# Performance work log

Measured on AMD Instinct MI355X. Metric: run time of the kernel, lower is better.

Reference implementation:

```python
import jax, jax.numpy as jnp
import numpy as np
import math

B, N, D, H = 2, 2048, 1024, 16
HD = D // H          # head dim = 64
ROT = 32             # rotary dim (applied to first ROT channels of each head)


def rotate_half(x):
    # '... (d r) -> ... d r' with r=2: even/odd interleaved pairs
    x1 = x[..., 0::2]
    x2 = x[..., 1::2]
    return jnp.stack((-x2, x1), axis=-1).reshape(x.shape)


def apply_rotary_pos_emb(t, freqs):
    rot_dim, seq_len = freqs.shape[-1], t.shape[-2]
    freqs = freqs[-seq_len:, :]
    t_rot, t_pass = t[..., :rot_dim], t[..., rot_dim:]
    t_rot = t_rot * jnp.cos(freqs) + rotate_half(t_rot) * jnp.sin(freqs)
    return jnp.concatenate((t_rot, t_pass), axis=-1)


def setup_inputs() -> dict:
    key = jax.random.key(0)
    ks = jax.random.split(key, 8)
    return {
        "q": jax.random.normal(ks[0], (B, N, D), jnp.float32),
        "k": jax.random.normal(ks[1], (B, N, D), jnp.float32),
        "v": jax.random.normal(ks[2], (B, N, D), jnp.float32),
        "wq": jax.random.normal(ks[3], (D, D), jnp.float32) * (1.0 / math.sqrt(D)),
        "wk": jax.random.normal(ks[4], (D, D), jnp.float32) * (1.0 / math.sqrt(D)),
        "wv": jax.random.normal(ks[5], (D, D), jnp.float32) * (1.0 / math.sqrt(D)),
        "wo": jax.random.normal(ks[6], (D, D), jnp.float32) * (1.0 / math.sqrt(D)),
        "rot_pos_emb": jax.random.normal(ks[7], (N, ROT), jnp.float32),
    }


def reference(q, k, v, wq, wk, wv, wo, rot_pos_emb):
    # projections (nn.Linear with bias=False: x @ W.T)
    qh = (q @ wq.T).reshape(B, N, H, HD).transpose(0, 2, 1, 3)  # b h n d
    kh = (k @ wk.T).reshape(B, N, H, HD).transpose(0, 2, 1, 3)
    vh = (v @ wv.T).reshape(B, N, H, HD).transpose(0, 2, 1, 3)
    qh = apply_rotary_pos_emb(qh, rot_pos_emb)
    kh = apply_rotary_pos_emb(kh, rot_pos_emb)
    k_t = kh.transpose(0, 1, 3, 2)                               # b h d n
    scores = (qh @ k_t) / math.sqrt(HD)                          # b h n n
    attn = jax.nn.softmax(scores, axis=-1)
    out = attn @ vh                                              # b h n d
    out = out.transpose(0, 2, 1, 3).reshape(B, N, H * HD)        # b n (h d)
    return (out @ wo.T, k_t, vh)
```

## Files before the change

### kernel.cpp

```cpp
#include <hip/hip_runtime.h>
#include <math.h>

#define NN 2048
#define DD 1024
#define HH 16
#define OUTSZ (2*NN*DD)

typedef unsigned short u16;
typedef unsigned int u32;
typedef __attribute__((ext_vector_type(8))) short short8;
typedef __attribute__((ext_vector_type(4))) float floatx4;
typedef __attribute__((ext_vector_type(4))) unsigned short us4;

__device__ __forceinline__ u16 f2bf(float x) {
    union { float f; unsigned u; } v; v.f = x;
    unsigned r = v.u + 0x7FFFu + ((v.u >> 16) & 1u);
    return (u16)(r >> 16);
}

__device__ __forceinline__ u32 fbits(float x) {
    union { float f; u32 u; } v; v.f = x; return v.u;
}

__device__ __forceinline__ u32 pack_bf2(float lo, float hi) {
    return __builtin_amdgcn_perm(fbits(hi) + 0x8000u, fbits(lo) + 0x8000u, 0x07060302u);
}

__device__ __forceinline__ float fexp2(float x) {
#if __has_builtin(__builtin_amdgcn_exp2f)
    return __builtin_amdgcn_exp2f(x);
#else
    return __expf(x * 0.69314718056f);
#endif
}

__device__ __forceinline__ void gl_lds16(const u16* g, u16* l) {
    __builtin_amdgcn_global_load_lds(
        (const __attribute__((address_space(1))) unsigned int*)g,
        (__attribute__((address_space(3))) unsigned int*)l, 16, 0, 0);
}

struct CastArgs { const float* s[7]; u16* d[7]; int n[7]; };

__global__ __launch_bounds__(256)
void cast_bf16(CastArgs a) {
    const int ten = blockIdx.y;
    const float4* s = (const float4*)a.s[ten];
    us4* d = (us4*)a.d[ten];
    const int n4 = a.n[ten] >> 2;
    for (int i = blockIdx.x * 256 + threadIdx.x; i < n4; i += gridDim.x * 256) {
        float4 f = s[i];
        us4 u = {f2bf(f.x), f2bf(f.y), f2bf(f.z), f2bf(f.w)};
        d[i] = u;
    }
}

struct ProjArgs {
    const u16* X[4]; const u16* W[4];
    float* outf[4];  u16* outb[4];
    const float* rot;
};

template<int TN>
__global__ __launch_bounds__(256)
void mfma_proj(ProjArgs a, int mode_base)
{
    constexpr int TNW = TN / 2;
    constexpr int NJ  = TNW / 16;

    __shared__ __align__(16) u16 As[128 * 64];
    __shared__ __align__(16) u16 Bs[TN * 64];

    const int mode = mode_base + blockIdx.z;
    const u16* __restrict__ X   = a.X[mode];
    const u16* __restrict__ Wm  = a.W[mode];
    float* __restrict__ outf    = a.outf[mode];
    u16* __restrict__ outb      = a.outb[mode];
    const float* __restrict__ rot = a.rot;

    const int t    = threadIdx.x;
    const int lane = t & 63;
    const int w    = t >> 6;
    const int wr   = (w >> 1) * 64;
    const int wc   = (w & 1) * TNW;
    const int m0   = blockIdx.y * 128;
    const int j0   = blockIdx.x * TN;

    const int lc = (t & 7) ^ ((t >> 3) & 7);
    const u16* gA = X  + (size_t)(m0 + (t >> 3)) * DD + lc * 8;
    const u16* gB = Wm + (size_t)(j0 + (t >> 3)) * DD + lc * 8;

    const int fr = lane & 15;
    const int fq = lane >> 4;

    floatx4 acc[4][NJ] = {};

    for (int k0 = 0; k0 < DD; k0 += 64) {
        __syncthreads();
        #pragma unroll
        for (int p = 0; p < 4; ++p)
            gl_lds16(gA + (size_t)(32 * p) * DD + k0, As + (p * 256 + t) * 8);
        #pragma unroll
        for (int p = 0; p < TN / 32; ++p)
            gl_lds16(gB + (size_t)(32 * p) * DD + k0, Bs + (p * 256 + t) * 8);
        __syncthreads();
        #pragma unroll
        for (int kk = 0; kk < 2; ++kk) {
            const int ph = (kk * 4 + fq) ^ (fr & 7);
            short8 af[4], bf[NJ];
            #pragma unroll
            for (int i = 0; i < 4; ++i)
                af[i] = *(const short8*)(As + (wr + i * 16 + fr) * 64 + ph * 8);
            #pragma unroll
            for (int j = 0; j < NJ; ++j)
                bf[j] = *(const short8*)(Bs + (wc + j * 16 + fr) * 64 + ph * 8);
            #pragma unroll
            for (int i = 0; i < 4; ++i)
                #pragma unroll
                for (int j = 0; j < NJ; ++j)
                    acc[i][j] = __builtin_amdgcn_mfma_f32_16x16x32_bf16(af[i], bf[j], acc[i][j], 0, 0, 0);
        }
    }

    const int b = m0 >> 11;
    #pragma unroll
    for (int i = 0; i < 4; ++i) {
        const int mrow  = m0 + wr + i * 16 + fq * 4;
        const int nbase = mrow & (NN - 1);
        #pragma unroll
        for (int j = 0; j < NJ; ++j) {
            const int col = j0 + wc + j * 16 + fr;
            const int h = col >> 6, d = col & 63;
            const int bh = b * HH + h;
            float v[4];
            #pragma unroll
            for (int r = 0; r < 4; ++r) v[r] = acc[i][j][r];
            if (mode <= 1 && ((wc + j * 16) & 63) < 32) {
                #pragma unroll
                for (int r = 0; r < 4; ++r) {
                    const int n = nbase + r;
                    float c = v[r];
                    float p = __shfl_xor(c, 1);
                    float f = rot[n * 32 + d];
                    float sn, cs; __sincosf(f, &sn, &cs);
                    v[r] = (d & 1) ? fmaf(c, cs, p * sn) : fmaf(c, cs, -p * sn);
                }
            }
            if (mode == 0) {
                #pragma unroll
                for (int r = 0; r < 4; ++r)
                    outb[((size_t)bh * NN + nbase + r) * 64 + d] = f2bf(v[r] * 0.1803368801111244f);
            } else if (mode == 1) {
                float4 f4 = {v[0], v[1], v[2], v[3]};
                *(float4*)&outf[((size_t)bh * 64 + d) * NN + nbase] = f4;
                #pragma unroll
                for (int r = 0; r < 4; ++r)
                    outb[((size_t)bh * NN + nbase + r) * 64 + d] = f2bf(v[r]);
            } else if (mode == 2) {
                #pragma unroll
                for (int r = 0; r < 4; ++r)
                    outf[((size_t)bh * NN + nbase + r) * 64 + d] = v[r];
                us4 u = {f2bf(v[0]), f2bf(v[1]), f2bf(v[2]), f2bf(v[3])};
                *(us4*)&outb[((size_t)bh * 64 + d) * NN + nbase] = u;
            } else {
                #pragma unroll
                for (int r = 0; r < 4; ++r)
                    outf[(size_t)(mrow + r) * DD + col] = v[r];
            }
        }
    }
}

__global__ __launch_bounds__(256)
void mfma_attn(const u16* __restrict__ qh, const u16* __restrict__ kh,
               const u16* __restrict__ vt, u16* __restrict__ ctx)
{
    __shared__ __align__(16) u16 Ks[64 * 64];
    __shared__ __align__(16) u16 Vs[64 * 64];
    __shared__ __align__(16) u16 Ps[4 * 32 * 64];

    const int t    = threadIdx.x;
    const int lane = t & 63;
    const int w    = t >> 6;
    const int fr   = lane & 15;
    const int fq   = lane >> 4;
    const int bh   = blockIdx.y;
    const int q0   = blockIdx.x * 128;
    const int b    = bh >> 4, h = bh & 15;

    short8 qf[2][2];
    #pragma unroll
    for (int c = 0; c < 2; ++c)
        #pragma unroll
        for (int kk = 0; kk < 2; ++kk)
            qf[c][kk] = *(const short8*)(qh +
                ((size_t)bh * NN + q0 + w * 32 + c * 16 + fr) * 64 + kk * 32 + fq * 8);

    const int lc = (t & 7) ^ ((t >> 3) & 7);
    const u16* kg = kh + ((size_t)bh * NN + (t >> 3)) * 64 + lc * 8;
    const u16* vg = vt + ((size_t)bh * 64 + (t >> 3)) * NN + lc * 8;
    u16* kl0 = Ks + t * 8;      u16* kl1 = Ks + (256 + t) * 8;
    u16* vl0 = Vs + t * 8;      u16* vl1 = Vs + (256 + t) * 8;

    u16* Prow0 = Ps + (w * 32 + fr) * 64;
    const int psw = 2 * (fr & 7);

    floatx4 o4[2][4] = {};
    float lrun[2] = {0.f, 0.f};

    for (int j0k = 0; j0k < NN; j0k += 64) {
        __syncthreads();
        gl_lds16(kg + (size_t)j0k * 64, kl0);
        gl_lds16(kg + (size_t)(j0k + 32) * 64, kl1);
        gl_lds16(vg + j0k, vl0);
        gl_lds16(vg + j0k + (size_t)32 * NN, vl1);
        __syncthreads();

        short8 kf[4][2];
        #pragma unroll
        for (int j = 0; j < 4; ++j)
            #pragma unroll
            for (int kk = 0; kk < 2; ++kk) {
                const int row = j * 16 + fr;
                const int phys = (kk * 4 + fq) ^ (row & 7);
                kf[j][kk] = *(const short8*)(Ks + row * 64 + phys * 8);
            }
        floatx4 sT[2][4] = {};
        #pragma unroll
        for (int c = 0; c < 2; ++c)
            #pragma unroll
            for (int j = 0; j < 4; ++j)
                #pragma unroll
                for (int kk = 0; kk < 2; ++kk)
                    sT[c][j] = __builtin_amdgcn_mfma_f32_16x16x32_bf16(kf[j][kk], qf[c][kk], sT[c][j], 0, 0, 0);

        #pragma unroll
        for (int c = 0; c < 2; ++c) {
            u16* pb = Prow0 + c * 16 * 64;
            #pragma unroll
            for (int j = 0; j < 4; ++j) {
                float p0 = fexp2(sT[c][j][0]);
                float p1 = fexp2(sT[c][j][1]);
                float p2 = fexp2(sT[c][j][2]);
                float p3 = fexp2(sT[c][j][3]);
                lrun[c] += (p0 + p1) + (p2 + p3);
                u32 lo = pack_bf2(p0, p1);
                u32 hi = pack_bf2(p2, p3);
                const int phys = (4 * j + fq) ^ psw;
                uint2 pv = {lo, hi};
                *(uint2*)(pb + phys * 4) = pv;
            }
        }

        short8 pa[2][2], vf[4][2];
        #pragma unroll
        for (int c = 0; c < 2; ++c)
            #pragma unroll
            for (int kk = 0; kk < 2; ++kk) {
                const int phys0 = (8 * kk + 2 * fq) ^ psw;
                pa[c][kk] = *(const short8*)(Prow0 + c * 16 * 64 + phys0 * 4);
            }
        #pragma unroll
        for (int n = 0; n < 4; ++n)
            #pragma unroll
            for (int kk = 0; kk < 2; ++kk) {
                const int row = n * 16 + fr;
                const int phys = (kk * 4 + fq) ^ (row & 7);
                vf[n][kk] = *(const short8*)(Vs + row * 64 + phys * 8);
            }
        #pragma unroll
        for (int c = 0; c < 2; ++c)
            #pragma unroll
            for (int n = 0; n < 4; ++n)
                #pragma unroll
                for (int kk = 0; kk < 2; ++kk)
                    o4[c][n] = __builtin_amdgcn_mfma_f32_16x16x32_bf16(pa[c][kk], vf[n][kk], o4[c][n], 0, 0, 0);
    }

    #pragma unroll
    for (int c = 0; c < 2; ++c) {
        lrun[c] += __shfl_xor(lrun[c], 16);
        lrun[c] += __shfl_xor(lrun[c], 32);
    }

    #pragma unroll
    for (int c = 0; c < 2; ++c)
        #pragma unroll
        for (int r = 0; r < 4; ++r) {
            const float inv = 1.0f / __shfl(lrun[c], fq * 4 + r);
            const int qrow = q0 + w * 32 + c * 16 + fq * 4 + r;
            const size_t base = ((size_t)b * NN + qrow) * DD + h * 64 + fr;
            #pragma unroll
            for (int n = 0; n < 4; ++n)
                ctx[base + n * 16] = f2bf(o4[c][n][r] * inv);
        }
}

extern "C" void kernel_launch(void* const* d_in, const int* in_sizes, int n_in,
                              void* d_out, int out_size, void* d_ws, size_t ws_size,
                              hipStream_t stream)
{
    const float* q   = (const float*)d_in[0];
    const float* k   = (const float*)d_in[1];
    const float* v   = (const float*)d_in[2];
    const float* wq  = (const float*)d_in[3];
    const float* wk  = (const float*)d_in[4];
    const float* wv  = (const float*)d_in[5];
    const float* wo  = (const float*)d_in[6];
    const float* rot = (const float*)d_in[7];

    float* out_final = (float*)d_out;
    float* out_kt    = out_final + OUTSZ;
    float* out_vh    = out_kt + OUTSZ;

    u16* wsb  = (u16*)d_ws;
    u16* qb   = wsb;
    u16* kb   = wsb + (size_t) 4 * 1024 * 1024;
    u16* vb   = wsb + (size_t) 8 * 1024 * 1024;
    u16* wqb  = wsb + (size_t)12 * 1024 * 1024;
    u16* wkb  = wsb + (size_t)13 * 1024 * 1024;
    u16* wvb  = wsb + (size_t)14 * 1024 * 1024;
    u16* wob  = wsb + (size_t)15 * 1024 * 1024;
    u16* qhb  = wsb + (size_t)16 * 1024 * 1024;
    u16* khb  = wsb + (size_t)20 * 1024 * 1024;
    u16* vtb  = wsb + (size_t)24 * 1024 * 1024;
    u16* ctxb = wsb + (size_t)28 * 1024 * 1024;

    CastArgs ca;
    ca.s[0] = q;  ca.d[0] = qb;  ca.n[0] = OUTSZ;
    ca.s[1] = k;  ca.d[1] = kb;  ca.n[1] = OUTSZ;
    ca.s[2] = v;  ca.d[2] = vb;  ca.n[2] = OUTSZ;
    ca.s[3] = wq; ca.d[3] = wqb; ca.n[3] = DD * DD;
    ca.s[4] = wk; ca.d[4] = wkb; ca.n[4] = DD * DD;
    ca.s[5] = wv; ca.d[5] = wvb; ca.n[5] = DD * DD;
    ca.s[6] = wo; ca.d[6] = wob; ca.n[6] = DD * DD;
    cast_bf16<<<dim3(256, 7), 256, 0, stream>>>(ca);

    ProjArgs pa;
    pa.X[0] = qb;   pa.W[0] = wqb; pa.outf[0] = nullptr;   pa.outb[0] = qhb;
    pa.X[1] = kb;   pa.W[1] = wkb; pa.outf[1] = out_kt;    pa.outb[1] = khb;
    pa.X[2] = vb;   pa.W[2] = wvb; pa.outf[2] = out_vh;    pa.outb[2] = vtb;
    pa.X[3] = ctxb; pa.W[3] = wob; pa.outf[3] = out_final; pa.outb[3] = nullptr;
    pa.rot = rot;

    mfma_proj<128><<<dim3(DD / 128, (2 * NN) / 128, 3), 256, 0, stream>>>(pa, 0);

    mfma_attn<<<dim3(NN / 128, 2 * HH), 256, 0, stream>>>(qhb, khb, vtb, ctxb);

    mfma_proj<64><<<dim3(DD / 64, (2 * NN) / 128, 1), 256, 0, stream>>>(pa, 3);
}
```

Measured before the change: 246.7 us.

## Split attention key dimension across waves with cross-wave output reduction

The attention kernel now gives each block 64 queries and processes 128 keys per iteration. Each of the four waves handles its own 32-key slice against all 64 queries, instead of each wave owning 32 queries against every key. Partial outputs and row sums are then reduced across waves through shared memory before a vectorized bf16 store. The grid is reordered so consecutive blocks share a head, which should improve K/V cache reuse, and launch bounds request 3 blocks per CU. In exchange, each wave carries more accumulator registers, and the final reduction is serialized over waves with several barriers.

```diff
diff --git a/kernel.cpp b/kernel.cpp
--- a/kernel.cpp
+++ b/kernel.cpp
@@ -171,129 +171,144 @@
     }
 }
 
-__global__ __launch_bounds__(256)
+__global__ __launch_bounds__(256, 3)
 void mfma_attn(const u16* __restrict__ qh, const u16* __restrict__ kh,
                const u16* __restrict__ vt, u16* __restrict__ ctx)
 {
-    __shared__ __align__(16) u16 Ks[64 * 64];
-    __shared__ __align__(16) u16 Vs[64 * 64];
-    __shared__ __align__(16) u16 Ps[4 * 32 * 64];
+    __shared__ __align__(16) u16 Ks[128 * 64];
+    __shared__ __align__(16) u16 Vs[64 * 128];
+    __shared__ __align__(16) u16 Ps[4 * 64 * 40];
+    __shared__ float Lsc[64];
 
     const int t    = threadIdx.x;
     const int lane = t & 63;
     const int w    = t >> 6;
     const int fr   = lane & 15;
     const int fq   = lane >> 4;
-    const int bh   = blockIdx.y;
-    const int q0   = blockIdx.x * 128;
+    const int bh   = blockIdx.x;
+    const int q0   = blockIdx.y * 64;
     const int b    = bh >> 4, h = bh & 15;
 
-    short8 qf[2][2];
+    short8 qf[4][2];
     #pragma unroll
-    for (int c = 0; c < 2; ++c)
+    for (int c = 0; c < 4; ++c)
         #pragma unroll
         for (int kk = 0; kk < 2; ++kk)
             qf[c][kk] = *(const short8*)(qh +
-                ((size_t)bh * NN + q0 + w * 32 + c * 16 + fr) * 64 + kk * 32 + fq * 8);
-
-    const int lc = (t & 7) ^ ((t >> 3) & 7);
-    const u16* kg = kh + ((size_t)bh * NN + (t >> 3)) * 64 + lc * 8;
-    const u16* vg = vt + ((size_t)bh * 64 + (t >> 3)) * NN + lc * 8;
-    u16* kl0 = Ks + t * 8;      u16* kl1 = Ks + (256 + t) * 8;
-    u16* vl0 = Vs + t * 8;      u16* vl1 = Vs + (256 + t) * 8;
-
-    u16* Prow0 = Ps + (w * 32 + fr) * 64;
-    const int psw = 2 * (fr & 7);
-
-    floatx4 o4[2][4] = {};
-    float lrun[2] = {0.f, 0.f};
-
-    for (int j0k = 0; j0k < NN; j0k += 64) {
-        __syncthreads();
-        gl_lds16(kg + (size_t)j0k * 64, kl0);
-        gl_lds16(kg + (size_t)(j0k + 32) * 64, kl1);
-        gl_lds16(vg + j0k, vl0);
-        gl_lds16(vg + j0k + (size_t)32 * NN, vl1);
-        __syncthreads();
-
-        short8 kf[4][2];
-        #pragma unroll
-        for (int j = 0; j < 4; ++j)
+                ((size_t)bh * NN + q0 + c * 16 + fr) * 64 + kk * 32 + fq * 8);
+
+    const int lc8  = (t & 7) ^ ((t >> 3) & 7);
+    const int lc16 = (t & 15) ^ ((t >> 4) & 15);
+    const u16* kg = kh + ((size_t)bh * NN + (t >> 3)) * 64 + lc8 * 8;
+    const u16* vg = vt + ((size_t)bh * 64 + (t >> 4)) * NN + lc16 * 8;
+
+    u16* Pw = Ps + w * 64 * 40;
+
+    floatx4 o4[4][4] = {};
+    float lrun[4] = {0.f, 0.f, 0.f, 0.f};
+
+    for (int j0k = 0; j0k < NN; j0k += 128) {
+        __syncthreads();
+        #pragma unroll
+        for (int p = 0; p < 4; ++p)
+            gl_lds16(kg + (size_t)(j0k + p * 32) * 64, Ks + (p * 256 + t) * 8);
+        #pragma unroll
+        for (int p = 0; p < 4; ++p)
+            gl_lds16(vg + (size_t)(p * 16) * NN + j0k, Vs + (p * 256 + t) * 8);
+        __syncthreads();
+
+        short8 kf[2][2];
+        #pragma unroll
+        for (int jt = 0; jt < 2; ++jt)
             #pragma unroll
             for (int kk = 0; kk < 2; ++kk) {
-                const int row = j * 16 + fr;
+                const int row = w * 32 + jt * 16 + fr;
                 const int phys = (kk * 4 + fq) ^ (row & 7);
-                kf[j][kk] = *(const short8*)(Ks + row * 64 + phys * 8);
+                kf[jt][kk] = *(const short8*)(Ks + row * 64 + phys * 8);
             }
         floatx4 sT[2][4] = {};
         #pragma unroll
-        for (int c = 0; c < 2; ++c)
-            #pragma unroll
-            for (int j = 0; j < 4; ++j)
+        for (int jt = 0; jt < 2; ++jt)
+            #pragma unroll
+            for (int c = 0; c < 4; ++c)
                 #pragma unroll
                 for (int kk = 0; kk < 2; ++kk)
-                    sT[c][j] = __builtin_amdgcn_mfma_f32_16x16x32_bf16(kf[j][kk], qf[c][kk], sT[c][j], 0, 0, 0);
-
-        #pragma unroll
-        for (int c = 0; c < 2; ++c) {
-            u16* pb = Prow0 + c * 16 * 64;
-            #pragma unroll
-            for (int j = 0; j < 4; ++j) {
-                float p0 = fexp2(sT[c][j][0]);
-                float p1 = fexp2(sT[c][j][1]);
-                float p2 = fexp2(sT[c][j][2]);
-                float p3 = fexp2(sT[c][j][3]);
+                    sT[jt][c] = __builtin_amdgcn_mfma_f32_16x16x32_bf16(kf[jt][kk], qf[c][kk], sT[jt][c], 0, 0, 0);
+
+        #pragma unroll
+        for (int c = 0; c < 4; ++c) {
+            u16* pb = Pw + (c * 16 + fr) * 40;
+            #pragma unroll
+            for (int jt = 0; jt < 2; ++jt) {
+                float p0 = fexp2(sT[jt][c][0]);
+                float p1 = fexp2(sT[jt][c][1]);
+                float p2 = fexp2(sT[jt][c][2]);
+                float p3 = fexp2(sT[jt][c][3]);
                 lrun[c] += (p0 + p1) + (p2 + p3);
-                u32 lo = pack_bf2(p0, p1);
-                u32 hi = pack_bf2(p2, p3);
-                const int phys = (4 * j + fq) ^ psw;
-                uint2 pv = {lo, hi};
-                *(uint2*)(pb + phys * 4) = pv;
-            }
-        }
-
-        short8 pa[2][2], vf[4][2];
-        #pragma unroll
-        for (int c = 0; c < 2; ++c)
-            #pragma unroll
-            for (int kk = 0; kk < 2; ++kk) {
-                const int phys0 = (8 * kk + 2 * fq) ^ psw;
-                pa[c][kk] = *(const short8*)(Prow0 + c * 16 * 64 + phys0 * 4);
-            }
-        #pragma unroll
-        for (int n = 0; n < 4; ++n)
-            #pragma unroll
-            for (int kk = 0; kk < 2; ++kk) {
-                const int row = n * 16 + fr;
-                const int phys = (kk * 4 + fq) ^ (row & 7);
-                vf[n][kk] = *(const short8*)(Vs + row * 64 + phys * 8);
-            }
-        #pragma unroll
-        for (int c = 0; c < 2; ++c)
+                uint2 pv = {pack_bf2(p0, p1), pack_bf2(p2, p3)};
+                *(uint2*)(pb + jt * 16 + fq * 4) = pv;
+            }
+        }
+
+        short8 pa[4], vf[4];
+        #pragma unroll
+        for (int m = 0; m < 4; ++m)
+            pa[m] = *(const short8*)(Pw + (m * 16 + fr) * 40 + fq * 8);
+        #pragma unroll
+        for (int n = 0; n < 4; ++n) {
+            const int row = n * 16 + fr;
+            const int phys = (w * 4 + fq) ^ (row & 15);
+            vf[n] = *(const short8*)(Vs + row * 128 + phys * 8);
+        }
+        #pragma unroll
+        for (int m = 0; m < 4; ++m)
             #pragma unroll
             for (int n = 0; n < 4; ++n)
-                #pragma unroll
-                for (int kk = 0; kk < 2; ++kk)
-                    o4[c][n] = __builtin_amdgcn_mfma_f32_16x16x32_bf16(pa[c][kk], vf[n][kk], o4[c][n], 0, 0, 0);
+                o4[m][n] = __builtin_amdgcn_mfma_f32_16x16x32_bf16(pa[m], vf[n], o4[m][n], 0, 0, 0);
     }
 
     #pragma unroll
-    for (int c = 0; c < 2; ++c) {
+    for (int c = 0; c < 4; ++c) {
         lrun[c] += __shfl_xor(lrun[c], 16);
         lrun[c] += __shfl_xor(lrun[c], 32);
     }
 
+    float* Osc = (float*)Ps;
+    __syncthreads();
+    for (int ww = 0; ww < 4; ++ww) {
+        if (w == ww) {
+            #pragma unroll
+            for (int m = 0; m < 4; ++m)
+                #pragma unroll
+                for (int n = 0; n < 4; ++n)
+                    #pragma unroll
+                    for (int r = 0; r < 4; ++r) {
+                        const int q = m * 16 + fq * 4 + r;
+                        const int d = n * 16 + fr;
+                        if (ww == 0) Osc[q * 64 + d] = o4[m][n][r];
+                        else         Osc[q * 64 + d] += o4[m][n][r];
+                    }
+            if (fq == 0) {
+                #pragma unroll
+                for (int c = 0; c < 4; ++c) {
+                    const int q = c * 16 + fr;
+                    if (ww == 0) Lsc[q] = lrun[c];
+                    else         Lsc[q] += lrun[c];
+                }
+            }
+        }
+        __syncthreads();
+    }
+
+    const int q  = t >> 2;
+    const float inv = 1.0f / Lsc[q];
     #pragma unroll
-    for (int c = 0; c < 2; ++c)
-        #pragma unroll
-        for (int r = 0; r < 4; ++r) {
-            const float inv = 1.0f / __shfl(lrun[c], fq * 4 + r);
-            const int qrow = q0 + w * 32 + c * 16 + fq * 4 + r;
-            const size_t base = ((size_t)b * NN + qrow) * DD + h * 64 + fr;
-            #pragma unroll
-            for (int n = 0; n < 4; ++n)
-                ctx[base + n * 16] = f2bf(o4[c][n][r] * inv);
-        }
+    for (int i = 0; i < 4; ++i) {
+        const int d0 = (t & 3) * 16 + i * 4;
+        float4 o = *(const float4*)(Osc + q * 64 + d0);
+        us4 u = {f2bf(o.x * inv), f2bf(o.y * inv), f2bf(o.z * inv), f2bf(o.w * inv)};
+        *(us4*)&ctx[((size_t)b * NN + q0 + q) * DD + h * 64 + d0] = u;
+    }
 }
 
 extern "C" void kernel_launch(void* const* d_in, const int* in_sizes, int n_in,
@@ -345,7 +360,7 @@
 
     mfma_proj<128><<<dim3(DD / 128, (2 * NN) / 128, 3), 256, 0, stream>>>(pa, 0);
 
-    mfma_attn<<<dim3(NN / 128, 2 * HH), 256, 0, stream>>>(qhb, khb, vtb, ctxb);
+    mfma_attn<<<dim3(2 * HH, NN / 64), 256, 0, stream>>>(qhb, khb, vtb, ctxb);
 
     mfma_proj<64><<<dim3(DD / 64, (2 * NN) / 128, 1), 256, 0, stream>>>(pa, 3);
 }
```

After: 242.3 us. Within noise of the previous version (-1.8%).
